# Kernel tuning notes

Measured on AMD Instinct MI355X. Metric: run time of the kernel, lower is better.

The kernel has to match this reference:

```python
import jax, jax.numpy as jnp
import numpy as np

N_NODES = 100000
N_EDGES = 1600000
IN_CH, HID_CH, OUT_CH = 64, 128, 64


def _sage_conv(x, src, dst, W_l, W_r, b):
    # PyG SAGEConv (mean aggr): out = lin_l(mean_{j in N(i)} x_j) + lin_r(x_i) + bias
    msg = x[src]  # [E, F] gather of source-node features
    agg_sum = jax.ops.segment_sum(msg, dst, num_segments=N_NODES)  # [N, F]
    cnt = jax.ops.segment_sum(jnp.ones((src.shape[0],), x.dtype), dst, num_segments=N_NODES)
    agg = agg_sum / jnp.maximum(cnt, 1.0)[:, None]  # mean; isolated nodes -> 0
    return agg @ W_l + x @ W_r + b


def setup_inputs() -> dict:
    key = jax.random.key(0)
    ks = jax.random.split(key, 8)
    x = jax.random.normal(ks[0], (N_NODES, IN_CH), dtype=jnp.float32)
    edge_index = jax.random.randint(ks[1], (2, N_EDGES), 0, N_NODES, dtype=jnp.int32)
    def glorot(k, shape):
        lim = float(np.sqrt(6.0 / (shape[0] + shape[1])))
        return jax.random.uniform(k, shape, jnp.float32, -lim, lim)
    W_l1 = glorot(ks[2], (IN_CH, HID_CH))
    W_r1 = glorot(ks[3], (IN_CH, HID_CH))
    b1 = jnp.zeros((HID_CH,), jnp.float32)
    W_l2 = glorot(ks[4], (HID_CH, OUT_CH))
    W_r2 = glorot(ks[5], (HID_CH, OUT_CH))
    b2 = jnp.zeros((OUT_CH,), jnp.float32)
    return {"x": x, "edge_index": edge_index, "W_l1": W_l1, "W_r1": W_r1, "b1": b1,
            "W_l2": W_l2, "W_r2": W_r2, "b2": b2}


def reference(x, edge_index, W_l1, W_r1, b1, W_l2, W_r2, b2):
    src, dst = edge_index[0], edge_index[1]
    h = jax.nn.relu(_sage_conv(x, src, dst, W_l1, W_r1, b1))
    out = _sage_conv(h, src, dst, W_l2, W_r2, b2)
    return jax.nn.sigmoid(out)
```

## Files before the change

kernel.cpp:

```cpp
#include <hip/hip_runtime.h>
#include <hip/hip_bf16.h>
#include <stdint.h>


#define NBMAX 784
#define BCAP 3584

typedef __bf16 bf16x8 __attribute__((ext_vector_type(8)));
typedef float f32x4 __attribute__((ext_vector_type(4)));

__device__ __forceinline__ float ldb(const unsigned short* p) {
  return __uint_as_float(((unsigned int)*p) << 16);
}

__device__ __forceinline__ unsigned short bf16u(float f) {
  __hip_bfloat16 h = __float2bfloat16(f);
  return *(unsigned short*)&h;
}

__global__ __launch_bounds__(256) void k_prep(const float* __restrict__ x,
                                              unsigned short* __restrict__ xb,
                                              const int* __restrict__ dst,
                                              unsigned int* __restrict__ hist,
                                              const float* __restrict__ Wl1,
                                              const float* __restrict__ Wr1,
                                              const float* __restrict__ Wl2,
                                              const float* __restrict__ Wr2,
                                              unsigned short* __restrict__ W1p,
                                              unsigned short* __restrict__ W2p,
                                              int N, int E, int NB, int castB, int histB) {
  __shared__ unsigned int lh[NBMAX];
  const int tid = threadIdx.x;
  const int b = blockIdx.x;
  if (b < castB) {
    int i = b * 256 + tid;
    if (i < N * 16) {
      int n = i >> 4, c4 = (i & 15) << 2;
      float4 v = *(const float4*)(x + (size_t)n * 64 + c4);
      unsigned int u0 = (unsigned int)bf16u(v.x) | ((unsigned int)bf16u(v.y) << 16);
      unsigned int u1 = (unsigned int)bf16u(v.z) | ((unsigned int)bf16u(v.w) << 16);
      *(uint2*)(xb + (size_t)n * 64 + c4) = make_uint2(u0, u1);
    }
  } else if (b < castB + histB) {
    for (int i = tid; i < NB; i += 256) lh[i] = 0;
    __syncthreads();
    const int e0 = (b - castB) * 16384;
    const int m = min(16384, E - e0);
    for (int i = tid; i < m; i += 256) atomicAdd(&lh[(unsigned int)dst[e0 + i] >> 7], 1u);
    __syncthreads();
    for (int i = tid; i < NB; i += 256) {
      unsigned int c = lh[i];
      if (c) atomicAdd(&hist[i], c);
    }
  } else {
    int f = (b - castB - histB) * 256 + tid;
    if (f < 4096) {
      int mat = f >> 11;
      int fr = f & 2047;
      int lane = fr & 63;
      int ntkb = fr >> 6;
      int nt = ntkb >> 2, kb = ntkb & 3;
      int col = (nt << 4) + (lane & 15);
      int k0 = (kb << 5) + ((lane >> 4) << 3);
      unsigned short v[8];
#pragma unroll
      for (int i = 0; i < 8; ++i) {
        int k = k0 + i;
        float val;
        if (mat == 0) val = (k < 64) ? Wl1[k * 128 + col] : Wr1[(k - 64) * 128 + col];
        else          val = (col < 64) ? Wl2[k * 64 + col] : Wr2[k * 64 + (col - 64)];
        v[i] = bf16u(val);
      }
      *(uint4*)((mat ? W2p : W1p) + (size_t)fr * 8) = *(const uint4*)v;
    }
  }
}

__global__ void k_scanb(const unsigned int* __restrict__ hist, unsigned int* __restrict__ base,
                        unsigned int* __restrict__ cursor, int NB) {
  const int lane = threadIdx.x;
  unsigned int running = 0;
  for (int b0 = 0; b0 < NB; b0 += 64) {
    int i = b0 + lane;
    unsigned int v = (i < NB) ? hist[i] : 0;
    unsigned int s = v;
#pragma unroll
    for (int off = 1; off < 64; off <<= 1) {
      unsigned int t = __shfl_up(s, off);
      if (lane >= off) s += t;
    }
    if (i < NB) {
      base[i] = running + s - v;
      cursor[i] = running + s - v;
    }
    running += __shfl(s, 63);
  }
  if (lane == 0) base[NB] = running;
}

__global__ __launch_bounds__(512) void k_part(const int* __restrict__ src,
                                              const int* __restrict__ dst,
                                              unsigned int* __restrict__ cursor,
                                              unsigned int* __restrict__ bkt, int E, int NB) {
  __shared__ unsigned int histL[NBMAX], lbase[NBMAX], gpos[NBMAX], lcur[NBMAX];
  __shared__ unsigned short stage[8192];
  const int tid = threadIdx.x;
  const int e0 = blockIdx.x * 8192;
  const int m = min(8192, E - e0);
  for (int b = tid; b < NB; b += 512) { histL[b] = 0; lcur[b] = 0; }
  __syncthreads();
  for (int i = tid; i < m; i += 512) atomicAdd(&histL[(unsigned int)dst[e0 + i] >> 7], 1u);
  __syncthreads();
  if (tid < 64) {
    unsigned int running = 0;
    for (int b0 = 0; b0 < NB; b0 += 64) {
      int i = b0 + tid;
      unsigned int v = (i < NB) ? histL[i] : 0;
      unsigned int s = v;
#pragma unroll
      for (int off = 1; off < 64; off <<= 1) {
        unsigned int t = __shfl_up(s, off);
        if (tid >= off) s += t;
      }
      if (i < NB) lbase[i] = running + s - v;
      running += __shfl(s, 63);
    }
  }
  __syncthreads();
  for (int b = tid; b < NB; b += 512) {
    unsigned int c = histL[b];
    gpos[b] = c ? atomicAdd(&cursor[b], c) : 0u;
  }
  for (int i = tid; i < m; i += 512) {
    unsigned int b = (unsigned int)dst[e0 + i] >> 7;
    unsigned int p = lbase[b] + atomicAdd(&lcur[b], 1u);
    stage[p] = (unsigned short)i;
  }
  __syncthreads();
  for (int i = tid; i < m; i += 512) {
    int idx = (int)stage[i];
    int d = dst[e0 + idx];
    int s = src[e0 + idx];
    unsigned int b = (unsigned int)d >> 7;
    bkt[gpos[b] + (unsigned int)i - lbase[b]] =
        (unsigned int)s | ((unsigned int)(d & 127) << 25);
  }
}

template <int EPI>
__global__ __launch_bounds__(512) void k_aggs(const unsigned short* __restrict__ feat,
                                              const unsigned int* __restrict__ bkt,
                                              const unsigned int* __restrict__ base,
                                              unsigned short* __restrict__ outRows,
                                              const float* __restrict__ z2,
                                              const float* __restrict__ b2,
                                              float* __restrict__ outF, int N) {
  __shared__ unsigned int pbufA[BCAP];
  __shared__ unsigned int pbufB[BCAP];
  __shared__ unsigned int hist[128], lofs[128], cur[128];
  const int tid = threadIdx.x;
  const int lane = tid & 63;
  const int w = tid >> 6;
  const int nodelo = blockIdx.x << 7;
  if (tid < 128) hist[tid] = 0;
  const int ebeg = (int)base[blockIdx.x];
  int m = (int)base[blockIdx.x + 1] - ebeg;
  m = (m > BCAP) ? BCAP : m;
  float bias = 0.f;
  if (EPI == 1) bias = b2[lane];
  __syncthreads();
  for (int i = tid; i < m; i += 512) {
    unsigned int t = bkt[ebeg + i];
    pbufA[i] = t;
    atomicAdd(&hist[t >> 25], 1u);
  }
  __syncthreads();
  if (tid < 64) {
    unsigned int v0 = hist[tid], v1 = hist[tid + 64];
    unsigned int s0 = v0, s1 = v1;
#pragma unroll
    for (int off = 1; off < 64; off <<= 1) {
      unsigned int t0 = __shfl_up(s0, off);
      unsigned int t1 = __shfl_up(s1, off);
      if (tid >= off) { s0 += t0; s1 += t1; }
    }
    unsigned int tot0 = __shfl(s0, 63);
    lofs[tid]      = s0 - v0;
    lofs[tid + 64] = tot0 + s1 - v1;
    cur[tid]       = s0 - v0;
    cur[tid + 64]  = tot0 + s1 - v1;
  }
  __syncthreads();
  for (int i = tid; i < m; i += 512) {
    unsigned int t = pbufA[i];
    unsigned int p = atomicAdd(&cur[t >> 25], 1u);
    pbufB[p] = t;
  }
  __syncthreads();
  for (int q = 0; q < 16; ++q) {
    const int r = (w << 4) + q;
    const int c = __builtin_amdgcn_readfirstlane((int)hist[r]);
    const int o = __builtin_amdgcn_readfirstlane((int)lofs[r]);
    float acc = 0.f;
    for (int e = 0; e < c; e += 16) {
      int si[16];
      float mk[16];
#pragma unroll
      for (int k = 0; k < 16; ++k) {
        int ee = e + k;
        int ec = (ee < c) ? ee : (c - 1);
        si[k] = __builtin_amdgcn_readfirstlane((int)(pbufB[o + ec] & 0x1FFFFFFu));
        mk[k] = (ee < c) ? 1.f : 0.f;
      }
      float f[16];
#pragma unroll
      for (int k = 0; k < 16; ++k) f[k] = ldb(feat + ((size_t)si[k] << 6) + lane);
#pragma unroll
      for (int k = 0; k < 16; ++k) acc = fmaf(f[k], mk[k], acc);
    }
    const int node = nodelo + r;
    if (node < N) {
      float sc = c ? (1.f / (float)c) : 0.f;
      float v = acc * sc;
      if (EPI == 0) {
        outRows[((size_t)node << 6) + lane] = bf16u(v);
      } else {
        float t = v + z2[((size_t)node << 6) + lane] + bias;
        outF[((size_t)node << 6) + lane] = 1.f / (1.f + __expf(-t));
      }
    }
  }
}

__global__ __launch_bounds__(256) void k_mmf(const unsigned short* __restrict__ agg,
                                             const unsigned short* __restrict__ xb,
                                             const unsigned short* __restrict__ W1p,
                                             const unsigned short* __restrict__ W2p,
                                             const float* __restrict__ b1,
                                             unsigned short* __restrict__ y2,
                                             float* __restrict__ z2, int N) {
  __shared__ __align__(16) unsigned short sH[64][136];
  __shared__ __align__(16) unsigned short sY[64][72];
  __shared__ __align__(16) float sZ[64][68];
  const int tid = threadIdx.x;
  const int lane = tid & 63;
  const int w = tid >> 6;
  const int n0 = blockIdx.x << 6;
  const int row16 = lane & 15;
  const int kgrp = lane >> 4;
  int node = n0 + (w << 4) + row16;
  if (node >= N) node = N - 1;

  bf16x8 a[4];
  {
    const unsigned short* ra = agg + ((size_t)node << 6);
    const unsigned short* rx = xb + ((size_t)node << 6);
    a[0] = *(const bf16x8*)(ra + kgrp * 8);
    a[1] = *(const bf16x8*)(ra + 32 + kgrp * 8);
    a[2] = *(const bf16x8*)(rx + kgrp * 8);
    a[3] = *(const bf16x8*)(rx + 32 + kgrp * 8);
  }
  const bf16x8* Wp1 = (const bf16x8*)W1p;
#pragma unroll
  for (int nt = 0; nt < 8; ++nt) {
    f32x4 acc = {0.f, 0.f, 0.f, 0.f};
#pragma unroll
    for (int kb = 0; kb < 4; ++kb) {
      bf16x8 b = Wp1[(nt * 4 + kb) * 64 + lane];
      acc = __builtin_amdgcn_mfma_f32_16x16x32_bf16(a[kb], b, acc, 0, 0, 0);
    }
    const int col = (nt << 4) + row16;
    const float bias = b1[col];
#pragma unroll
    for (int r = 0; r < 4; ++r) {
      int lrow = (w << 4) + (kgrp << 2) + r;
      sH[lrow][col] = bf16u(fmaxf(acc[r] + bias, 0.f));
    }
  }
  __syncthreads();
  bf16x8 h4[4];
  {
    const int hr = (w << 4) + row16;
#pragma unroll
    for (int kb = 0; kb < 4; ++kb)
      h4[kb] = *(const bf16x8*)(&sH[hr][kb * 32 + kgrp * 8]);
  }
  const bf16x8* Wp2 = (const bf16x8*)W2p;
#pragma unroll
  for (int nt = 0; nt < 8; ++nt) {
    f32x4 acc = {0.f, 0.f, 0.f, 0.f};
#pragma unroll
    for (int kb = 0; kb < 4; ++kb) {
      bf16x8 b = Wp2[(nt * 4 + kb) * 64 + lane];
      acc = __builtin_amdgcn_mfma_f32_16x16x32_bf16(h4[kb], b, acc, 0, 0, 0);
    }
    const int col = (nt << 4) + row16;
#pragma unroll
    for (int r = 0; r < 4; ++r) {
      int lrow = (w << 4) + (kgrp << 2) + r;
      if (nt < 4) sY[lrow][col] = bf16u(acc[r]);
      else        sZ[lrow][col - 64] = acc[r];
    }
  }
  __syncthreads();
#pragma unroll
  for (int it = 0; it < 2; ++it) {
    int idx = it * 256 + tid;
    int r = idx >> 3, sub = idx & 7;
    int nn = n0 + r;
    if (nn < N)
      *(uint4*)((char*)(y2 + ((size_t)nn << 6)) + sub * 16) =
          *(const uint4*)((char*)&sY[r][0] + sub * 16);
  }
#pragma unroll
  for (int it = 0; it < 4; ++it) {
    int idx = it * 256 + tid;
    int r = idx >> 4, sub = idx & 15;
    int nn = n0 + r;
    if (nn < N)
      *(uint4*)((char*)(z2 + ((size_t)nn << 6)) + sub * 16) =
          *(const uint4*)((char*)&sZ[r][0] + sub * 16);
  }
}

extern "C" void kernel_launch(void* const* d_in, const int* in_sizes, int n_in,
                              void* d_out, int out_size, void* d_ws, size_t ws_size,
                              hipStream_t stream) {
  const float* x   = (const float*)d_in[0];
  const int*   ei  = (const int*)d_in[1];
  const float* Wl1 = (const float*)d_in[2];
  const float* Wr1 = (const float*)d_in[3];
  const float* b1  = (const float*)d_in[4];
  const float* Wl2 = (const float*)d_in[5];
  const float* Wr2 = (const float*)d_in[6];
  const float* b2  = (const float*)d_in[7];
  float* out = (float*)d_out;

  const int N = in_sizes[0] / 64;
  const int E = in_sizes[1] / 2;
  int NB = (N + 127) >> 7;
  if (NB > NBMAX) NB = NBMAX;
  const int* src = ei;
  const int* dst = ei + E;

  char* wp = (char*)d_ws;
  auto take = [&](size_t bytes) {
    char* p = wp;
    wp += (bytes + 255) & ~(size_t)255;
    return p;
  };
  unsigned int* hist   = (unsigned int*)take((size_t)NBMAX * 4);
  unsigned int* base   = (unsigned int*)take((size_t)(NBMAX + 1) * 4);
  unsigned int* cursor = (unsigned int*)take((size_t)NBMAX * 4);
  unsigned int* bkt    = (unsigned int*)take((size_t)E * 4);
  unsigned short* W1p  = (unsigned short*)take(128 * 128 * 2);
  unsigned short* W2p  = (unsigned short*)take(128 * 128 * 2);
  unsigned short* xb   = (unsigned short*)take((size_t)N * 64 * 2);
  unsigned short* agg  = (unsigned short*)take((size_t)N * 64 * 2);
  unsigned short* y2   = (unsigned short*)take((size_t)N * 64 * 2);
  float* z2            = (float*)take((size_t)N * 64 * 4);

  hipMemsetAsync(hist, 0, (size_t)NBMAX * 4, stream);

  const int castB = (N * 16 + 255) / 256;
  const int histB = (E + 16383) / 16384;
  k_prep<<<castB + histB + 16, 256, 0, stream>>>(x, xb, dst, hist, Wl1, Wr1, Wl2, Wr2,
                                                 W1p, W2p, N, E, NB, castB, histB);
  k_scanb<<<1, 64, 0, stream>>>(hist, base, cursor, NB);
  k_part<<<(E + 8191) / 8192, 512, 0, stream>>>(src, dst, cursor, bkt, E, NB);

  const int nb64 = (N + 63) / 64;
  k_aggs<0><<<NB, 512, 0, stream>>>(xb, bkt, base, agg, nullptr, nullptr, nullptr, N);
  k_mmf<<<nb64, 256, 0, stream>>>(agg, xb, W1p, W2p, b1, y2, z2, N);
  k_aggs<1><<<NB, 512, 0, stream>>>(y2, bkt, base, nullptr, z2, b2, out, N);
}
```

Measured before the change: 290.2 us.

## Persist per-block sorted buckets and degrees for second aggregation; unroll gather loop

The first aggregation pass now writes the locally sorted edge bucket back to global memory and stores per-node degrees, so the second pass skips the histogram and counting sort and only re-scans the degrees. The gather loop also changes from padded 16-wide masked FMAs to exact-count unrolled chunks of 8, 4 and 1 with plain adds. This saves LDS atomics and barriers in layer 2 at the cost of extra global writes in layer 1 and an extra degs buffer.

Result: faster. 252.3 us (-13.0%).

```diff
diff --git a/kernel.cpp b/kernel.cpp
--- a/kernel.cpp
+++ b/kernel.cpp
@@ -149,8 +149,9 @@
 
 template <int EPI>
 __global__ __launch_bounds__(512) void k_aggs(const unsigned short* __restrict__ feat,
-                                              const unsigned int* __restrict__ bkt,
+                                              unsigned int* __restrict__ bkt,
                                               const unsigned int* __restrict__ base,
+                                              unsigned int* __restrict__ degs,
                                               unsigned short* __restrict__ outRows,
                                               const float* __restrict__ z2,
                                               const float* __restrict__ b2,
@@ -162,61 +163,104 @@
   const int lane = tid & 63;
   const int w = tid >> 6;
   const int nodelo = blockIdx.x << 7;
-  if (tid < 128) hist[tid] = 0;
   const int ebeg = (int)base[blockIdx.x];
   int m = (int)base[blockIdx.x + 1] - ebeg;
   m = (m > BCAP) ? BCAP : m;
   float bias = 0.f;
   if (EPI == 1) bias = b2[lane];
-  __syncthreads();
-  for (int i = tid; i < m; i += 512) {
-    unsigned int t = bkt[ebeg + i];
-    pbufA[i] = t;
-    atomicAdd(&hist[t >> 25], 1u);
-  }
-  __syncthreads();
-  if (tid < 64) {
-    unsigned int v0 = hist[tid], v1 = hist[tid + 64];
-    unsigned int s0 = v0, s1 = v1;
-#pragma unroll
-    for (int off = 1; off < 64; off <<= 1) {
-      unsigned int t0 = __shfl_up(s0, off);
-      unsigned int t1 = __shfl_up(s1, off);
-      if (tid >= off) { s0 += t0; s1 += t1; }
-    }
-    unsigned int tot0 = __shfl(s0, 63);
-    lofs[tid]      = s0 - v0;
-    lofs[tid + 64] = tot0 + s1 - v1;
-    cur[tid]       = s0 - v0;
-    cur[tid + 64]  = tot0 + s1 - v1;
-  }
-  __syncthreads();
-  for (int i = tid; i < m; i += 512) {
-    unsigned int t = pbufA[i];
-    unsigned int p = atomicAdd(&cur[t >> 25], 1u);
-    pbufB[p] = t;
-  }
-  __syncthreads();
+
+  if (EPI == 0) {
+    if (tid < 128) hist[tid] = 0;
+    __syncthreads();
+    for (int i = tid; i < m; i += 512) {
+      unsigned int t = bkt[ebeg + i];
+      pbufA[i] = t;
+      atomicAdd(&hist[t >> 25], 1u);
+    }
+    __syncthreads();
+    if (tid < 64) {
+      unsigned int v0 = hist[tid], v1 = hist[tid + 64];
+      unsigned int s0 = v0, s1 = v1;
+#pragma unroll
+      for (int off = 1; off < 64; off <<= 1) {
+        unsigned int t0 = __shfl_up(s0, off);
+        unsigned int t1 = __shfl_up(s1, off);
+        if (tid >= off) { s0 += t0; s1 += t1; }
+      }
+      unsigned int tot0 = __shfl(s0, 63);
+      lofs[tid]      = s0 - v0;
+      lofs[tid + 64] = tot0 + s1 - v1;
+      cur[tid]       = s0 - v0;
+      cur[tid + 64]  = tot0 + s1 - v1;
+    }
+    __syncthreads();
+    for (int i = tid; i < m; i += 512) {
+      unsigned int t = pbufA[i];
+      unsigned int p = atomicAdd(&cur[t >> 25], 1u);
+      pbufB[p] = t;
+    }
+    __syncthreads();
+    for (int i = tid; i < m; i += 512) bkt[ebeg + i] = pbufB[i];
+    if (tid < 128) degs[nodelo + tid] = hist[tid];
+  } else {
+    if (tid < 128) hist[tid] = degs[nodelo + tid];
+    for (int i = tid; i < m; i += 512) pbufB[i] = bkt[ebeg + i];
+    __syncthreads();
+    if (tid < 64) {
+      unsigned int v0 = hist[tid], v1 = hist[tid + 64];
+      unsigned int s0 = v0, s1 = v1;
+#pragma unroll
+      for (int off = 1; off < 64; off <<= 1) {
+        unsigned int t0 = __shfl_up(s0, off);
+        unsigned int t1 = __shfl_up(s1, off);
+        if (tid >= off) { s0 += t0; s1 += t1; }
+      }
+      unsigned int tot0 = __shfl(s0, 63);
+      lofs[tid]      = s0 - v0;
+      lofs[tid + 64] = tot0 + s1 - v1;
+    }
+    __syncthreads();
+  }
+
   for (int q = 0; q < 16; ++q) {
     const int r = (w << 4) + q;
-    const int c = __builtin_amdgcn_readfirstlane((int)hist[r]);
-    const int o = __builtin_amdgcn_readfirstlane((int)lofs[r]);
+    const unsigned int c = hist[r];
+    const unsigned int o = lofs[r];
     float acc = 0.f;
-    for (int e = 0; e < c; e += 16) {
-      int si[16];
-      float mk[16];
-#pragma unroll
-      for (int k = 0; k < 16; ++k) {
-        int ee = e + k;
-        int ec = (ee < c) ? ee : (c - 1);
-        si[k] = __builtin_amdgcn_readfirstlane((int)(pbufB[o + ec] & 0x1FFFFFFu));
-        mk[k] = (ee < c) ? 1.f : 0.f;
-      }
-      float f[16];
-#pragma unroll
-      for (int k = 0; k < 16; ++k) f[k] = ldb(feat + ((size_t)si[k] << 6) + lane);
-#pragma unroll
-      for (int k = 0; k < 16; ++k) acc = fmaf(f[k], mk[k], acc);
+    unsigned int e = 0;
+    for (; e + 8 <= c; e += 8) {
+      int s0 = __builtin_amdgcn_readfirstlane((int)(pbufB[o + e + 0] & 0x1FFFFFFu));
+      int s1 = __builtin_amdgcn_readfirstlane((int)(pbufB[o + e + 1] & 0x1FFFFFFu));
+      int s2 = __builtin_amdgcn_readfirstlane((int)(pbufB[o + e + 2] & 0x1FFFFFFu));
+      int s3 = __builtin_amdgcn_readfirstlane((int)(pbufB[o + e + 3] & 0x1FFFFFFu));
+      int s4 = __builtin_amdgcn_readfirstlane((int)(pbufB[o + e + 4] & 0x1FFFFFFu));
+      int s5 = __builtin_amdgcn_readfirstlane((int)(pbufB[o + e + 5] & 0x1FFFFFFu));
+      int s6 = __builtin_amdgcn_readfirstlane((int)(pbufB[o + e + 6] & 0x1FFFFFFu));
+      int s7 = __builtin_amdgcn_readfirstlane((int)(pbufB[o + e + 7] & 0x1FFFFFFu));
+      float f0 = ldb(feat + ((size_t)s0 << 6) + lane);
+      float f1 = ldb(feat + ((size_t)s1 << 6) + lane);
+      float f2 = ldb(feat + ((size_t)s2 << 6) + lane);
+      float f3 = ldb(feat + ((size_t)s3 << 6) + lane);
+      float f4 = ldb(feat + ((size_t)s4 << 6) + lane);
+      float f5 = ldb(feat + ((size_t)s5 << 6) + lane);
+      float f6 = ldb(feat + ((size_t)s6 << 6) + lane);
+      float f7 = ldb(feat + ((size_t)s7 << 6) + lane);
+      acc += f0 + f1 + f2 + f3 + f4 + f5 + f6 + f7;
+    }
+    for (; e + 4 <= c; e += 4) {
+      int s0 = __builtin_amdgcn_readfirstlane((int)(pbufB[o + e + 0] & 0x1FFFFFFu));
+      int s1 = __builtin_amdgcn_readfirstlane((int)(pbufB[o + e + 1] & 0x1FFFFFFu));
+      int s2 = __builtin_amdgcn_readfirstlane((int)(pbufB[o + e + 2] & 0x1FFFFFFu));
+      int s3 = __builtin_amdgcn_readfirstlane((int)(pbufB[o + e + 3] & 0x1FFFFFFu));
+      float f0 = ldb(feat + ((size_t)s0 << 6) + lane);
+      float f1 = ldb(feat + ((size_t)s1 << 6) + lane);
+      float f2 = ldb(feat + ((size_t)s2 << 6) + lane);
+      float f3 = ldb(feat + ((size_t)s3 << 6) + lane);
+      acc += f0 + f1 + f2 + f3;
+    }
+    for (; e < c; ++e) {
+      int s0 = __builtin_amdgcn_readfirstlane((int)(pbufB[o + e] & 0x1FFFFFFu));
+      acc += ldb(feat + ((size_t)s0 << 6) + lane);
     }
     const int node = nodelo + r;
     if (node < N) {
@@ -353,6 +397,7 @@
   unsigned int* base   = (unsigned int*)take((size_t)(NBMAX + 1) * 4);
   unsigned int* cursor = (unsigned int*)take((size_t)NBMAX * 4);
   unsigned int* bkt    = (unsigned int*)take((size_t)E * 4);
+  unsigned int* degs   = (unsigned int*)take((size_t)NBMAX * 128 * 4);
   unsigned short* W1p  = (unsigned short*)take(128 * 128 * 2);
   unsigned short* W2p  = (unsigned short*)take(128 * 128 * 2);
   unsigned short* xb   = (unsigned short*)take((size_t)N * 64 * 2);
@@ -370,7 +415,7 @@
   k_part<<<(E + 8191) / 8192, 512, 0, stream>>>(src, dst, cursor, bkt, E, NB);
 
   const int nb64 = (N + 63) / 64;
-  k_aggs<0><<<NB, 512, 0, stream>>>(xb, bkt, base, agg, nullptr, nullptr, nullptr, N);
+  k_aggs<0><<<NB, 512, 0, stream>>>(xb, bkt, base, degs, agg, nullptr, nullptr, nullptr, N);
   k_mmf<<<nb64, 256, 0, stream>>>(agg, xb, W1p, W2p, b1, y2, z2, N);
-  k_aggs<1><<<NB, 512, 0, stream>>>(y2, bkt, base, nullptr, z2, b2, out, N);
-}
+  k_aggs<1><<<NB, 512, 0, stream>>>(y2, bkt, base, degs, nullptr, z2, b2, out, N);
+}
```
